# Kernel optimization log

Measured on AMD Instinct MI355X. Metric: run time of the kernel, lower is better.

Reference implementation:

```python
import jax, jax.numpy as jnp
import numpy as np

N_NODES = 100000
N_EDGES = 1600000
IN_DIM, HID, OUT_DIM = 128, 64, 1


def _sage_conv(x, src, dst, wl, wr, b, num_nodes):
    # PyG SAGEConv (aggr='mean', root_weight=True):
    #   out = lin_l(mean_{j in N(i)} x_j) + lin_r(x_i), bias lives in lin_l
    msgs = x[src]                                                  # [E, d] gather
    agg = jax.ops.segment_sum(msgs, dst, num_segments=num_nodes)  # [N, d]
    deg = jax.ops.segment_sum(jnp.ones((src.shape[0],), x.dtype), dst,
                              num_segments=num_nodes)              # [N]
    agg = agg / jnp.maximum(deg, 1.0)[:, None]                     # mean aggregation
    return agg @ wl + x @ wr + b


def setup_inputs() -> dict:
    key = jax.random.key(0)
    ks = jax.random.split(key, 12)
    x = jax.random.normal(ks[0], (N_NODES, IN_DIM), dtype=jnp.float32)
    edge_index = jax.random.randint(ks[1], (2, N_EDGES), 0, N_NODES, dtype=jnp.int64)

    def glorot(k, fan_in, fan_out):
        s = jnp.sqrt(2.0 / (fan_in + fan_out)).astype(jnp.float32)
        return jax.random.normal(k, (fan_in, fan_out), dtype=jnp.float32) * s

    return {
        "x": x,
        "edge_index": edge_index,
        "wl0": glorot(ks[2], IN_DIM, HID), "wr0": glorot(ks[3], IN_DIM, HID),
        "b0": jnp.zeros((HID,), jnp.float32),
        "wl1": glorot(ks[4], HID, HID), "wr1": glorot(ks[5], HID, HID),
        "b1": jnp.zeros((HID,), jnp.float32),
        "wl2": glorot(ks[6], HID, OUT_DIM), "wr2": glorot(ks[7], HID, OUT_DIM),
        "b2": jnp.zeros((OUT_DIM,), jnp.float32),
    }


def reference(x, edge_index, wl0, wr0, b0, wl1, wr1, b1, wl2, wr2, b2):
    src, dst = edge_index[0], edge_index[1]
    n = x.shape[0]
    # layer 0: conv -> relu (dropout is identity in eval mode)
    h = jax.nn.relu(_sage_conv(x, src, dst, wl0, wr0, b0, n))
    # layer 1
    h = jax.nn.relu(_sage_conv(h, src, dst, wl1, wr1, b1, n))
    # final layer + sigmoid
    h = _sage_conv(h, src, dst, wl2, wr2, b2, n)
    return jax.nn.sigmoid(h)
```

## Files before the change

### kernel.cpp

```cpp
#include <hip/hip_runtime.h>
#include <hip/hip_bf16.h>
#include <math.h>


#define SHIFT 7
#define BKT 128
#define CHUNK 4096
#define CAP 4096
#define HSTR 72

typedef __bf16 bf16_t;
typedef bf16_t bf16x8 __attribute__((ext_vector_type(8)));
typedef float f32x4 __attribute__((ext_vector_type(4)));

#define B16LO(u) __uint_as_float((u) << 16)
#define B16HI(u) __uint_as_float((u) & 0xffff0000u)

__global__ __launch_bounds__(256) void scatter_prep(const int* __restrict__ srcv,
                                                    const int* __restrict__ dstv,
                                                    int* __restrict__ bcnt,
                                                    int* __restrict__ bucketed,
                                                    int E, int NB, int nbC,
                                                    const float* __restrict__ wl0,
                                                    const float* __restrict__ wr0,
                                                    const float* __restrict__ wl1,
                                                    const float* __restrict__ wr1,
                                                    bf16_t* __restrict__ w0t,
                                                    bf16_t* __restrict__ w1t) {
    if ((int)blockIdx.x >= nbC) {
        int idx = (blockIdx.x - nbC) * 256 + threadIdx.x;
        if (idx < 128 * 128) {
            int j = idx >> 7, k = idx & 127;
            float v = (j < 64) ? wl0[k * 64 + j] : wr0[k * 64 + (j - 64)];
            w0t[idx] = (bf16_t)v;
        } else if (idx < 128 * 128 + 128 * 64) {
            int i2 = idx - 128 * 128;
            int j = i2 >> 6, k = i2 & 63;
            float v = (j < 64) ? wl1[k * 64 + j] : wr1[k * 64 + (j - 64)];
            w1t[i2] = (bf16_t)v;
        }
        return;
    }
    __shared__ int hist[1024];
    __shared__ int offl[1024];
    __shared__ int basel[1024];
    __shared__ int partial[256];
    __shared__ int posA[CHUNK];
    __shared__ int valA[CHUNK];
    const int t = threadIdx.x;
    for (int i = t; i < NB; i += 256) hist[i] = 0;
    __syncthreads();

    const int cbase = blockIdx.x * CHUNK;
    int bk[CHUNK / 256], rk[CHUNK / 256], vv[CHUNK / 256];
#pragma unroll
    for (int k = 0; k < CHUNK / 256; ++k) {
        int e = cbase + t + k * 256;
        if (e < E) {
            int d = dstv[e];
            int s = srcv[e];
            int b = d >> SHIFT;
            bk[k] = b;
            rk[k] = atomicAdd(&hist[b], 1);
            vv[k] = (s << SHIFT) | (d & (BKT - 1));
        } else {
            bk[k] = -1;
        }
    }
    __syncthreads();

    for (int b = t; b < NB; b += 256) {
        int c = hist[b];
        basel[b] = c ? (b * CAP + atomicAdd(&bcnt[b], c)) : 0;
    }
    {
        int g = t * 4;
        int a0 = (g + 0 < NB) ? hist[g + 0] : 0;
        int a1 = (g + 1 < NB) ? hist[g + 1] : 0;
        int a2 = (g + 2 < NB) ? hist[g + 2] : 0;
        int a3 = (g + 3 < NB) ? hist[g + 3] : 0;
        int sum = a0 + a1 + a2 + a3;
        partial[t] = sum;
        __syncthreads();
        for (int d = 1; d < 256; d <<= 1) {
            int x = (t >= d) ? partial[t - d] : 0;
            __syncthreads();
            partial[t] += x;
            __syncthreads();
        }
        int ex = partial[t] - sum;
        if (g + 0 < NB) offl[g + 0] = ex;
        if (g + 1 < NB) offl[g + 1] = ex + a0;
        if (g + 2 < NB) offl[g + 2] = ex + a0 + a1;
        if (g + 3 < NB) offl[g + 3] = ex + a0 + a1 + a2;
    }
    __syncthreads();

    int nloc = E - cbase;
    if (nloc > CHUNK) nloc = CHUNK;
#pragma unroll
    for (int k = 0; k < CHUNK / 256; ++k) {
        if (bk[k] >= 0) {
            int slot = offl[bk[k]] + rk[k];
            posA[slot] = basel[bk[k]] + rk[k];
            valA[slot] = vv[k];
        }
    }
    __syncthreads();
    for (int j = t; j < nloc; j += 256) bucketed[posA[j]] = valA[j];
}

__global__ __launch_bounds__(256) void sort_gemm0(const int* __restrict__ bucketed,
                                                  const int* __restrict__ bcnt,
                                                  int2* __restrict__ od,
                                                  int* __restrict__ csr, int N, int NB,
                                                  const float* __restrict__ x,
                                                  const bf16_t* __restrict__ w0t,
                                                  bf16_t* __restrict__ y) {
    __shared__ int cnt[BKT];
    __shared__ int sc[BKT];
    __shared__ int cur[BKT];
    const int t = threadIdx.x;

    if ((int)blockIdx.x >= NB) {
        const int bid = blockIdx.x - NB;
        const int lane = t & 63;
        const int wv = t >> 6;
        const int r0 = bid * 64 + wv * 16;
        const int rr = lane & 15;
        const int quad = lane >> 4;
        const int row_store = r0 + rr;
        int row = (row_store < N) ? row_store : (N - 1);

        bf16x8 xf[4];
#pragma unroll
        for (int kk = 0; kk < 4; ++kk) {
            const float* ap = &x[(size_t)row * 128 + kk * 32 + quad * 8];
            float4 f0 = *(const float4*)ap;
            float4 f1 = *(const float4*)(ap + 4);
            union { bf16x8 v; bf16_t h[8]; } u;
            u.h[0] = (bf16_t)f0.x; u.h[1] = (bf16_t)f0.y;
            u.h[2] = (bf16_t)f0.z; u.h[3] = (bf16_t)f0.w;
            u.h[4] = (bf16_t)f1.x; u.h[5] = (bf16_t)f1.y;
            u.h[6] = (bf16_t)f1.z; u.h[7] = (bf16_t)f1.w;
            xf[kk] = u.v;
        }
#pragma unroll
        for (int c = 0; c < 8; ++c) {
            f32x4 acc = {0.f, 0.f, 0.f, 0.f};
#pragma unroll
            for (int kk = 0; kk < 4; ++kk) {
                bf16x8 wf = *(const bf16x8*)&w0t[(size_t)(c * 16 + rr) * 128 + kk * 32 + quad * 8];
                acc = __builtin_amdgcn_mfma_f32_16x16x32_bf16(wf, xf[kk], acc, 0, 0, 0);
            }
            if (row_store < N) {
                union { bf16_t h[4]; uint2 u; } p;
                p.h[0] = (bf16_t)acc[0]; p.h[1] = (bf16_t)acc[1];
                p.h[2] = (bf16_t)acc[2]; p.h[3] = (bf16_t)acc[3];
                *(uint2*)&y[(size_t)row_store * 128 + c * 16 + quad * 4] = p.u;
            }
        }
        return;
    }

    const int b = blockIdx.x;
    const int ebase = b * CAP;
    const int eend = ebase + bcnt[b];
    if (t < BKT) cnt[t] = 0;
    __syncthreads();
    int wreg[CAP / 256];
#pragma unroll
    for (int k = 0; k < CAP / 256; ++k) {
        int i = ebase + t + k * 256;
        if (i < eend) {
            wreg[k] = bucketed[i];
            atomicAdd(&cnt[wreg[k] & (BKT - 1)], 1);
        }
    }
    __syncthreads();
    int v = (t < BKT) ? cnt[t] : 0;
    if (t < BKT) sc[t] = v;
    __syncthreads();
    for (int d = 1; d < BKT; d <<= 1) {
        int xsc = (t < BKT && t >= d) ? sc[t - d] : 0;
        __syncthreads();
        if (t < BKT) sc[t] += xsc;
        __syncthreads();
    }
    if (t < BKT) {
        int ex = sc[t] - v;
        cur[t] = ex;
        int dst = (b << SHIFT) + t;
        if (dst < N) od[dst] = make_int2(ebase + ex, v);
    }
    __syncthreads();
#pragma unroll
    for (int k = 0; k < CAP / 256; ++k) {
        int i = ebase + t + k * 256;
        if (i < eend) {
            int w = wreg[k];
            int p = atomicAdd(&cur[w & (BKT - 1)], 1);
            csr[ebase + p] = w >> SHIFT;
        }
    }
}

__global__ __launch_bounds__(256) void agg0_gemm1(const bf16_t* __restrict__ y,
                                                  const int* __restrict__ csr,
                                                  const int2* __restrict__ od,
                                                  const float* __restrict__ bias,
                                                  const bf16_t* __restrict__ w1t,
                                                  bf16_t* __restrict__ Y, int N) {
    __shared__ bf16_t hlds[64 * HSTR];
    const int t = threadIdx.x;
    const int lane = t & 63;
    const int wv = t >> 6;
    const int oct = lane >> 3;
    const int ch = (lane & 7) * 8;
    const int gbase = blockIdx.x * 64;
    const int n0 = gbase + wv * 16;

    const float4 bv0 = *(const float4*)&bias[ch];
    const float4 bv1 = *(const float4*)&bias[ch + 4];

    int i = n0;
    int2 odc = (i < N) ? od[i] : make_int2(0, 0);
    int sidx = 0;
    if (i < N && lane < odc.y) sidx = csr[odc.x + lane];

    for (int k = 0; k < 16; ++k) {
        const int inext = n0 + k + 1;
        const bool pf = (k < 15) && (inext < N);
        int2 odn = pf ? od[inext] : make_int2(0, 0);

        const int base = odc.x;
        const int d = (i < N) ? odc.y : 0;
        float a0 = 0.f, a1 = 0.f, a2 = 0.f, a3 = 0.f;
        float a4 = 0.f, a5 = 0.f, a6 = 0.f, a7 = 0.f;
        const int nblk = d >> 3;
        const int pm = (nblk < 8) ? nblk : 8;
        int p = 0;
        for (; p + 2 <= pm; p += 2) {
            int s0 = __shfl(sidx, 8 * p + oct);
            int s1 = __shfl(sidx, 8 * p + 8 + oct);
            uint4 v0 = *(const uint4*)&y[(size_t)s0 * 128 + ch];
            uint4 v1 = *(const uint4*)&y[(size_t)s1 * 128 + ch];
            a0 += B16LO(v0.x) + B16LO(v1.x); a1 += B16HI(v0.x) + B16HI(v1.x);
            a2 += B16LO(v0.y) + B16LO(v1.y); a3 += B16HI(v0.y) + B16HI(v1.y);
            a4 += B16LO(v0.z) + B16LO(v1.z); a5 += B16HI(v0.z) + B16HI(v1.z);
            a6 += B16LO(v0.w) + B16LO(v1.w); a7 += B16HI(v0.w) + B16HI(v1.w);
        }
        for (; p < pm; ++p) {
            int s0 = __shfl(sidx, 8 * p + oct);
            uint4 v0 = *(const uint4*)&y[(size_t)s0 * 128 + ch];
            a0 += B16LO(v0.x); a1 += B16HI(v0.x);
            a2 += B16LO(v0.y); a3 += B16HI(v0.y);
            a4 += B16LO(v0.z); a5 += B16HI(v0.z);
            a6 += B16LO(v0.w); a7 += B16HI(v0.w);
        }
        for (; p < nblk; ++p) {
            int s0 = csr[base + 8 * p + oct];
            uint4 v0 = *(const uint4*)&y[(size_t)s0 * 128 + ch];
            a0 += B16LO(v0.x); a1 += B16HI(v0.x);
            a2 += B16LO(v0.y); a3 += B16HI(v0.y);
            a4 += B16LO(v0.z); a5 += B16HI(v0.z);
            a6 += B16LO(v0.w); a7 += B16HI(v0.w);
        }
        {
            int te = 8 * nblk + oct;
            int tec = (te < 64) ? te : 63;
            int s_t = __shfl(sidx, tec);
            if (te < d) {
                int s0 = (te < 64) ? s_t : csr[base + te];
                uint4 v0 = *(const uint4*)&y[(size_t)s0 * 128 + ch];
                a0 += B16LO(v0.x); a1 += B16HI(v0.x);
                a2 += B16LO(v0.y); a3 += B16HI(v0.y);
                a4 += B16LO(v0.z); a5 += B16HI(v0.z);
                a6 += B16LO(v0.w); a7 += B16HI(v0.w);
            }
        }

        int sidxn = 0;
        if (pf && lane < odn.y) sidxn = csr[odn.x + lane];

        a0 += __shfl_xor(a0, 8);  a1 += __shfl_xor(a1, 8);
        a2 += __shfl_xor(a2, 8);  a3 += __shfl_xor(a3, 8);
        a4 += __shfl_xor(a4, 8);  a5 += __shfl_xor(a5, 8);
        a6 += __shfl_xor(a6, 8);  a7 += __shfl_xor(a7, 8);
        a0 += __shfl_xor(a0, 16); a1 += __shfl_xor(a1, 16);
        a2 += __shfl_xor(a2, 16); a3 += __shfl_xor(a3, 16);
        a4 += __shfl_xor(a4, 16); a5 += __shfl_xor(a5, 16);
        a6 += __shfl_xor(a6, 16); a7 += __shfl_xor(a7, 16);
        a0 += __shfl_xor(a0, 32); a1 += __shfl_xor(a1, 32);
        a2 += __shfl_xor(a2, 32); a3 += __shfl_xor(a3, 32);
        a4 += __shfl_xor(a4, 32); a5 += __shfl_xor(a5, 32);
        a6 += __shfl_xor(a6, 32); a7 += __shfl_xor(a7, 32);

        if (i < N) {
            float inv = 1.f / ((d > 0) ? (float)d : 1.f);
            uint4 vs = *(const uint4*)&y[(size_t)i * 128 + 64 + ch];
            float v0 = fmaxf(a0 * inv + B16LO(vs.x) + bv0.x, 0.f);
            float v1 = fmaxf(a1 * inv + B16HI(vs.x) + bv0.y, 0.f);
            float v2 = fmaxf(a2 * inv + B16LO(vs.y) + bv0.z, 0.f);
            float v3 = fmaxf(a3 * inv + B16HI(vs.y) + bv0.w, 0.f);
            float v4 = fmaxf(a4 * inv + B16LO(vs.z) + bv1.x, 0.f);
            float v5 = fmaxf(a5 * inv + B16HI(vs.z) + bv1.y, 0.f);
            float v6 = fmaxf(a6 * inv + B16LO(vs.w) + bv1.z, 0.f);
            float v7 = fmaxf(a7 * inv + B16HI(vs.w) + bv1.w, 0.f);
            if (oct == 0) {
                union { bf16_t b[8]; uint4 u; } pk;
                pk.b[0] = (bf16_t)v0; pk.b[1] = (bf16_t)v1;
                pk.b[2] = (bf16_t)v2; pk.b[3] = (bf16_t)v3;
                pk.b[4] = (bf16_t)v4; pk.b[5] = (bf16_t)v5;
                pk.b[6] = (bf16_t)v6; pk.b[7] = (bf16_t)v7;
                *(uint4*)&hlds[(wv * 16 + k) * HSTR + ch] = pk.u;
            }
        }

        odc = odn;
        sidx = sidxn;
        i = inext;
    }
    __syncthreads();

    const int rr = lane & 15;
    const int quad = lane >> 4;
    const int row_store = gbase + wv * 16 + rr;

    bf16x8 xf[2];
#pragma unroll
    for (int kk = 0; kk < 2; ++kk)
        xf[kk] = *(const bf16x8*)&hlds[(wv * 16 + rr) * HSTR + kk * 32 + quad * 8];

#pragma unroll
    for (int c = 0; c < 8; ++c) {
        f32x4 acc = {0.f, 0.f, 0.f, 0.f};
#pragma unroll
        for (int kk = 0; kk < 2; ++kk) {
            bf16x8 wf = *(const bf16x8*)&w1t[(size_t)(c * 16 + rr) * 64 + kk * 32 + quad * 8];
            acc = __builtin_amdgcn_mfma_f32_16x16x32_bf16(wf, xf[kk], acc, 0, 0, 0);
        }
        if (row_store < N) {
            union { bf16_t h[4]; uint2 u; } p;
            p.h[0] = (bf16_t)acc[0]; p.h[1] = (bf16_t)acc[1];
            p.h[2] = (bf16_t)acc[2]; p.h[3] = (bf16_t)acc[3];
            *(uint2*)&Y[(size_t)row_store * 128 + c * 16 + quad * 4] = p.u;
        }
    }
}

__global__ __launch_bounds__(256) void agg1(const bf16_t* __restrict__ y,
                                            const int* __restrict__ csr,
                                            const int2* __restrict__ od,
                                            const float* __restrict__ bias,
                                            const float* __restrict__ wl2,
                                            const float* __restrict__ wr2,
                                            float* __restrict__ sl,
                                            float* __restrict__ sr, int N) {
    const int lane = threadIdx.x & 63;
    const int oct = lane >> 3;
    const int ch = (lane & 7) * 8;
    const int nw = gridDim.x * 4;

    int i = blockIdx.x * 4 + (threadIdx.x >> 6);
    int2 odc = (i < N) ? od[i] : make_int2(0, 0);
    int sidx = 0;
    if (i < N) sidx = (lane < odc.y) ? csr[odc.x + lane] : 0;

    while (i < N) {
        const int inext = i + nw;
        int2 odn = (inext < N) ? od[inext] : make_int2(0, 0);

        const int base = odc.x;
        const int d = odc.y;
        float a0 = 0.f, a1 = 0.f, a2 = 0.f, a3 = 0.f;
        float a4 = 0.f, a5 = 0.f, a6 = 0.f, a7 = 0.f;
        const int nblk = d >> 3;
        const int pm = (nblk < 8) ? nblk : 8;
        int p = 0;
        for (; p + 2 <= pm; p += 2) {
            int s0 = __shfl(sidx, 8 * p + oct);
            int s1 = __shfl(sidx, 8 * p + 8 + oct);
            uint4 v0 = *(const uint4*)&y[(size_t)s0 * 128 + ch];
            uint4 v1 = *(const uint4*)&y[(size_t)s1 * 128 + ch];
            a0 += B16LO(v0.x) + B16LO(v1.x); a1 += B16HI(v0.x) + B16HI(v1.x);
            a2 += B16LO(v0.y) + B16LO(v1.y); a3 += B16HI(v0.y) + B16HI(v1.y);
            a4 += B16LO(v0.z) + B16LO(v1.z); a5 += B16HI(v0.z) + B16HI(v1.z);
            a6 += B16LO(v0.w) + B16LO(v1.w); a7 += B16HI(v0.w) + B16HI(v1.w);
        }
        for (; p < pm; ++p) {
            int s0 = __shfl(sidx, 8 * p + oct);
            uint4 v0 = *(const uint4*)&y[(size_t)s0 * 128 + ch];
            a0 += B16LO(v0.x); a1 += B16HI(v0.x);
            a2 += B16LO(v0.y); a3 += B16HI(v0.y);
            a4 += B16LO(v0.z); a5 += B16HI(v0.z);
            a6 += B16LO(v0.w); a7 += B16HI(v0.w);
        }
        for (; p < nblk; ++p) {
            int s0 = csr[base + 8 * p + oct];
            uint4 v0 = *(const uint4*)&y[(size_t)s0 * 128 + ch];
            a0 += B16LO(v0.x); a1 += B16HI(v0.x);
            a2 += B16LO(v0.y); a3 += B16HI(v0.y);
            a4 += B16LO(v0.z); a5 += B16HI(v0.z);
            a6 += B16LO(v0.w); a7 += B16HI(v0.w);
        }
        {
            int te = 8 * nblk + oct;
            int tec = (te < 64) ? te : 63;
            int s_t = __shfl(sidx, tec);
            if (te < d) {
                int s0 = (te < 64) ? s_t : csr[base + te];
                uint4 v0 = *(const uint4*)&y[(size_t)s0 * 128 + ch];
                a0 += B16LO(v0.x); a1 += B16HI(v0.x);
                a2 += B16LO(v0.y); a3 += B16HI(v0.y);
                a4 += B16LO(v0.z); a5 += B16HI(v0.z);
                a6 += B16LO(v0.w); a7 += B16HI(v0.w);
            }
        }

        int sidxn = 0;
        if (inext < N) sidxn = (lane < odn.y) ? csr[odn.x + lane] : 0;

        a0 += __shfl_xor(a0, 8);  a1 += __shfl_xor(a1, 8);
        a2 += __shfl_xor(a2, 8);  a3 += __shfl_xor(a3, 8);
        a4 += __shfl_xor(a4, 8);  a5 += __shfl_xor(a5, 8);
        a6 += __shfl_xor(a6, 8);  a7 += __shfl_xor(a7, 8);
        a0 += __shfl_xor(a0, 16); a1 += __shfl_xor(a1, 16);
        a2 += __shfl_xor(a2, 16); a3 += __shfl_xor(a3, 16);
        a4 += __shfl_xor(a4, 16); a5 += __shfl_xor(a5, 16);
        a6 += __shfl_xor(a6, 16); a7 += __shfl_xor(a7, 16);
        a0 += __shfl_xor(a0, 32); a1 += __shfl_xor(a1, 32);
        a2 += __shfl_xor(a2, 32); a3 += __shfl_xor(a3, 32);
        a4 += __shfl_xor(a4, 32); a5 += __shfl_xor(a5, 32);
        a6 += __shfl_xor(a6, 32); a7 += __shfl_xor(a7, 32);

        float inv = 1.f / ((d > 0) ? (float)d : 1.f);
        uint4 vs = *(const uint4*)&y[(size_t)i * 128 + 64 + ch];
        float4 bv0 = *(const float4*)&bias[ch];
        float4 bv1 = *(const float4*)&bias[ch + 4];
        float v0 = fmaxf(a0 * inv + B16LO(vs.x) + bv0.x, 0.f);
        float v1 = fmaxf(a1 * inv + B16HI(vs.x) + bv0.y, 0.f);
        float v2 = fmaxf(a2 * inv + B16LO(vs.y) + bv0.z, 0.f);
        float v3 = fmaxf(a3 * inv + B16HI(vs.y) + bv0.w, 0.f);
        float v4 = fmaxf(a4 * inv + B16LO(vs.z) + bv1.x, 0.f);
        float v5 = fmaxf(a5 * inv + B16HI(vs.z) + bv1.y, 0.f);
        float v6 = fmaxf(a6 * inv + B16LO(vs.w) + bv1.z, 0.f);
        float v7 = fmaxf(a7 * inv + B16HI(vs.w) + bv1.w, 0.f);

        {
            float4 w0 = *(const float4*)&wl2[ch];
            float4 w1 = *(const float4*)&wl2[ch + 4];
            float4 u0 = *(const float4*)&wr2[ch];
            float4 u1 = *(const float4*)&wr2[ch + 4];
            float a = v0 * w0.x + v1 * w0.y + v2 * w0.z + v3 * w0.w +
                      v4 * w1.x + v5 * w1.y + v6 * w1.z + v7 * w1.w;
            float b = v0 * u0.x + v1 * u0.y + v2 * u0.z + v3 * u0.w +
                      v4 * u1.x + v5 * u1.y + v6 * u1.z + v7 * u1.w;
            a += __shfl_xor(a, 1); b += __shfl_xor(b, 1);
            a += __shfl_xor(a, 2); b += __shfl_xor(b, 2);
            a += __shfl_xor(a, 4); b += __shfl_xor(b, 4);
            if (lane == 0) { sl[i] = a; sr[i] = b; }
        }

        odc = odn;
        sidx = sidxn;
        i = inext;
    }
}

__global__ __launch_bounds__(256) void final_k(const float* __restrict__ sl,
                                               const float* __restrict__ sr,
                                               const int* __restrict__ csr,
                                               const int2* __restrict__ od,
                                               const float* __restrict__ b2,
                                               float* __restrict__ out, int N) {
    int wid = blockIdx.x * 4 + (threadIdx.x >> 6);
    if (wid >= N) return;
    const int lane = threadIdx.x & 63;
    const int2 odv = od[wid];
    const int base = odv.x;
    const int d = odv.y;
    float acc = 0.f;
    for (int e = lane; e < d; e += 64) acc += sl[csr[base + e]];
#pragma unroll
    for (int off = 32; off; off >>= 1) acc += __shfl_xor(acc, off);
    if (lane == 0) {
        float m = (d > 0) ? (float)d : 1.f;
        float v = acc / m + sr[wid] + b2[0];
        out[wid] = 1.f / (1.f + expf(-v));
    }
}

extern "C" void kernel_launch(void* const* d_in, const int* in_sizes, int n_in,
                              void* d_out, int out_size, void* d_ws, size_t ws_size,
                              hipStream_t stream) {
    const float* x  = (const float*)d_in[0];
    const int*  ei  = (const int*)d_in[1];
    const float* wl0 = (const float*)d_in[2];
    const float* wr0 = (const float*)d_in[3];
    const float* b0  = (const float*)d_in[4];
    const float* wl1 = (const float*)d_in[5];
    const float* wr1 = (const float*)d_in[6];
    const float* b1  = (const float*)d_in[7];
    const float* wl2 = (const float*)d_in[8];
    const float* wr2 = (const float*)d_in[9];
    const float* b2  = (const float*)d_in[10];
    float* out = (float*)d_out;

    const int E = in_sizes[1] / 2;
    const int N = out_size;
    const int* srcv = ei;
    const int* dstv = ei + E;
    const int NB = (N + BKT - 1) >> SHIFT;

    char* ws = (char*)d_ws;
    size_t o = 0;
    auto take = [&](size_t nbytes) -> void* {
        void* p = ws + o;
        o = (o + nbytes + 255) & ~(size_t)255;
        return p;
    };
    int2* od      = (int2*)take((size_t)N * 8);
    int* bcnt     = (int*)take((size_t)(NB + 2) * 4);
    int* bucketed = (int*)take((size_t)NB * CAP * 4);
    int* csr      = (int*)take((size_t)NB * CAP * 4);
    bf16_t* w0t   = (bf16_t*)take(128 * 128 * 2);
    bf16_t* w1t   = (bf16_t*)take(128 * 64 * 2);
    bf16_t* y     = (bf16_t*)take((size_t)N * 128 * 2);
    bf16_t* y2    = (bf16_t*)take((size_t)N * 128 * 2);
    float* sl     = (float*)take((size_t)N * 4);
    float* sr     = (float*)take((size_t)N * 4);
    (void)ws_size;

    const int nbC = (E + CHUNK - 1) / CHUNK;
    const int nbP = (128 * 128 + 128 * 64 + 255) / 256;
    const int nbW = (N + 3) / 4;
    const int nbG = (N + 63) / 64;
    const int nbA = 2048;

    hipMemsetAsync(bcnt, 0, (size_t)NB * 4, stream);
    scatter_prep<<<nbC + nbP, 256, 0, stream>>>(srcv, dstv, bcnt, bucketed, E, NB, nbC,
                                                wl0, wr0, wl1, wr1, w0t, w1t);
    sort_gemm0<<<NB + nbG, 256, 0, stream>>>(bucketed, bcnt, od, csr, N, NB,
                                             x, w0t, y);

    agg0_gemm1<<<nbG, 256, 0, stream>>>(y, csr, od, b0, w1t, y2, N);
    agg1<<<nbA, 256, 0, stream>>>(y2, csr, od, b1, wl2, wr2, sl, sr, N);
    final_k<<<nbW, 256, 0, stream>>>(sl, sr, csr, od, b2, out, N);
}
```

Measured before the change: 290.2 us.

## Fuse per-bucket sort with layer-0 aggregation and layer-1 GEMM, cache CSR in LDS

The kernel pipeline is reorganized. Weight conversion and the bucket-count zeroing move into a small init kernel that replaces the memset. The layer-0 GEMM now runs in the same launch as the edge scatter. The per-bucket counting sort is fused with layer-0 mean aggregation and the layer-1 MFMA GEMM, so each block builds its 128 destinations' CSR and keeps the first 2560 entries in shared memory for the gather. This removes one launch and the CSR/offset round trip through global memory. In exchange, larger shared memory per block may lower occupancy, and the aggregation now has only NB blocks of parallelism, 128 nodes each.

Measured after the change: 289.7 us. No clear change (-0.2%).

```diff
diff --git a/kernel.cpp b/kernel.cpp
--- a/kernel.cpp
+++ b/kernel.cpp
@@ -7,6 +7,7 @@
 #define BKT 128
 #define CHUNK 4096
 #define CAP 4096
+#define LCAP 2560
 #define HSTR 72
 
 typedef __bf16 bf16_t;
@@ -16,31 +17,90 @@
 #define B16LO(u) __uint_as_float((u) << 16)
 #define B16HI(u) __uint_as_float((u) & 0xffff0000u)
 
-__global__ __launch_bounds__(256) void scatter_prep(const int* __restrict__ srcv,
-                                                    const int* __restrict__ dstv,
-                                                    int* __restrict__ bcnt,
-                                                    int* __restrict__ bucketed,
-                                                    int E, int NB, int nbC,
-                                                    const float* __restrict__ wl0,
-                                                    const float* __restrict__ wr0,
-                                                    const float* __restrict__ wl1,
-                                                    const float* __restrict__ wr1,
-                                                    bf16_t* __restrict__ w0t,
-                                                    bf16_t* __restrict__ w1t) {
+#define ADD8(P, V) { P##0 += B16LO(V.x); P##1 += B16HI(V.x); \
+                     P##2 += B16LO(V.y); P##3 += B16HI(V.y); \
+                     P##4 += B16LO(V.z); P##5 += B16HI(V.z); \
+                     P##6 += B16LO(V.w); P##7 += B16HI(V.w); }
+#define BFLY(P, M) { P##0 += __shfl_xor(P##0, M); P##1 += __shfl_xor(P##1, M); \
+                     P##2 += __shfl_xor(P##2, M); P##3 += __shfl_xor(P##3, M); \
+                     P##4 += __shfl_xor(P##4, M); P##5 += __shfl_xor(P##5, M); \
+                     P##6 += __shfl_xor(P##6, M); P##7 += __shfl_xor(P##7, M); }
+
+__global__ __launch_bounds__(256) void init_k(const float* __restrict__ wl0,
+                                              const float* __restrict__ wr0,
+                                              const float* __restrict__ wl1,
+                                              const float* __restrict__ wr1,
+                                              bf16_t* __restrict__ w0t,
+                                              bf16_t* __restrict__ w1t,
+                                              int* __restrict__ bcnt,
+                                              int NB, int nbP) {
+    if ((int)blockIdx.x >= nbP) {
+        for (int i = threadIdx.x; i < NB; i += 256) bcnt[i] = 0;
+        return;
+    }
+    int idx = blockIdx.x * 256 + threadIdx.x;
+    if (idx < 128 * 128) {
+        int j = idx >> 7, k = idx & 127;
+        float v = (j < 64) ? wl0[k * 64 + j] : wr0[k * 64 + (j - 64)];
+        w0t[idx] = (bf16_t)v;
+    } else if (idx < 128 * 128 + 128 * 64) {
+        int i2 = idx - 128 * 128;
+        int j = i2 >> 6, k = i2 & 63;
+        float v = (j < 64) ? wl1[k * 64 + j] : wr1[k * 64 + (j - 64)];
+        w1t[i2] = (bf16_t)v;
+    }
+}
+
+__global__ __launch_bounds__(256) void scatter_gemm0(const int* __restrict__ srcv,
+                                                     const int* __restrict__ dstv,
+                                                     int* __restrict__ bcnt,
+                                                     int* __restrict__ bucketed,
+                                                     int E, int NB, int nbC,
+                                                     const float* __restrict__ x,
+                                                     const bf16_t* __restrict__ w0t,
+                                                     bf16_t* __restrict__ y, int N) {
     if ((int)blockIdx.x >= nbC) {
-        int idx = (blockIdx.x - nbC) * 256 + threadIdx.x;
-        if (idx < 128 * 128) {
-            int j = idx >> 7, k = idx & 127;
-            float v = (j < 64) ? wl0[k * 64 + j] : wr0[k * 64 + (j - 64)];
-            w0t[idx] = (bf16_t)v;
-        } else if (idx < 128 * 128 + 128 * 64) {
-            int i2 = idx - 128 * 128;
-            int j = i2 >> 6, k = i2 & 63;
-            float v = (j < 64) ? wl1[k * 64 + j] : wr1[k * 64 + (j - 64)];
-            w1t[i2] = (bf16_t)v;
+        const int bid = blockIdx.x - nbC;
+        const int t = threadIdx.x;
+        const int lane = t & 63;
+        const int wv = t >> 6;
+        const int r0 = bid * 64 + wv * 16;
+        const int rr = lane & 15;
+        const int quad = lane >> 4;
+        const int row_store = r0 + rr;
+        int row = (row_store < N) ? row_store : (N - 1);
+
+        bf16x8 xf[4];
+#pragma unroll
+        for (int kk = 0; kk < 4; ++kk) {
+            const float* ap = &x[(size_t)row * 128 + kk * 32 + quad * 8];
+            float4 f0 = *(const float4*)ap;
+            float4 f1 = *(const float4*)(ap + 4);
+            union { bf16x8 v; bf16_t h[8]; } u;
+            u.h[0] = (bf16_t)f0.x; u.h[1] = (bf16_t)f0.y;
+            u.h[2] = (bf16_t)f0.z; u.h[3] = (bf16_t)f0.w;
+            u.h[4] = (bf16_t)f1.x; u.h[5] = (bf16_t)f1.y;
+            u.h[6] = (bf16_t)f1.z; u.h[7] = (bf16_t)f1.w;
+            xf[kk] = u.v;
+        }
+#pragma unroll
+        for (int c = 0; c < 8; ++c) {
+            f32x4 acc = {0.f, 0.f, 0.f, 0.f};
+#pragma unroll
+            for (int kk = 0; kk < 4; ++kk) {
+                bf16x8 wf = *(const bf16x8*)&w0t[(size_t)(c * 16 + rr) * 128 + kk * 32 + quad * 8];
+                acc = __builtin_amdgcn_mfma_f32_16x16x32_bf16(wf, xf[kk], acc, 0, 0, 0);
+            }
+            if (row_store < N) {
+                union { bf16_t h[4]; uint2 u; } p;
+                p.h[0] = (bf16_t)acc[0]; p.h[1] = (bf16_t)acc[1];
+                p.h[2] = (bf16_t)acc[2]; p.h[3] = (bf16_t)acc[3];
+                *(uint2*)&y[(size_t)row_store * 128 + c * 16 + quad * 4] = p.u;
+            }
         }
         return;
     }
+
     __shared__ int hist[1024];
     __shared__ int offl[1024];
     __shared__ int basel[1024];
@@ -83,9 +143,9 @@
         partial[t] = sum;
         __syncthreads();
         for (int d = 1; d < 256; d <<= 1) {
-            int x = (t >= d) ? partial[t - d] : 0;
+            int xsc = (t >= d) ? partial[t - d] : 0;
             __syncthreads();
-            partial[t] += x;
+            partial[t] += xsc;
             __syncthreads();
         }
         int ex = partial[t] - sum;
@@ -110,62 +170,26 @@
     for (int j = t; j < nloc; j += 256) bucketed[posA[j]] = valA[j];
 }
 
-__global__ __launch_bounds__(256) void sort_gemm0(const int* __restrict__ bucketed,
-                                                  const int* __restrict__ bcnt,
-                                                  int2* __restrict__ od,
-                                                  int* __restrict__ csr, int N, int NB,
-                                                  const float* __restrict__ x,
-                                                  const bf16_t* __restrict__ w0t,
-                                                  bf16_t* __restrict__ y) {
+__global__ __launch_bounds__(256) void sort_agg0_gemm1(const int* __restrict__ bucketed,
+                                                       const int* __restrict__ bcnt,
+                                                       int2* __restrict__ od,
+                                                       int* __restrict__ csr,
+                                                       const bf16_t* __restrict__ y,
+                                                       const float* __restrict__ bias,
+                                                       const bf16_t* __restrict__ w1t,
+                                                       bf16_t* __restrict__ y2,
+                                                       int N, int NB) {
     __shared__ int cnt[BKT];
     __shared__ int sc[BKT];
     __shared__ int cur[BKT];
+    __shared__ int lcsr[LCAP];
+    __shared__ bf16_t hlds[BKT * HSTR];
     const int t = threadIdx.x;
-
-    if ((int)blockIdx.x >= NB) {
-        const int bid = blockIdx.x - NB;
-        const int lane = t & 63;
-        const int wv = t >> 6;
-        const int r0 = bid * 64 + wv * 16;
-        const int rr = lane & 15;
-        const int quad = lane >> 4;
-        const int row_store = r0 + rr;
-        int row = (row_store < N) ? row_store : (N - 1);
-
-        bf16x8 xf[4];
-#pragma unroll
-        for (int kk = 0; kk < 4; ++kk) {
-            const float* ap = &x[(size_t)row * 128 + kk * 32 + quad * 8];
-            float4 f0 = *(const float4*)ap;
-            float4 f1 = *(const float4*)(ap + 4);
-            union { bf16x8 v; bf16_t h[8]; } u;
-            u.h[0] = (bf16_t)f0.x; u.h[1] = (bf16_t)f0.y;
-            u.h[2] = (bf16_t)f0.z; u.h[3] = (bf16_t)f0.w;
-            u.h[4] = (bf16_t)f1.x; u.h[5] = (bf16_t)f1.y;
-            u.h[6] = (bf16_t)f1.z; u.h[7] = (bf16_t)f1.w;
-            xf[kk] = u.v;
-        }
-#pragma unroll
-        for (int c = 0; c < 8; ++c) {
-            f32x4 acc = {0.f, 0.f, 0.f, 0.f};
-#pragma unroll
-            for (int kk = 0; kk < 4; ++kk) {
-                bf16x8 wf = *(const bf16x8*)&w0t[(size_t)(c * 16 + rr) * 128 + kk * 32 + quad * 8];
-                acc = __builtin_amdgcn_mfma_f32_16x16x32_bf16(wf, xf[kk], acc, 0, 0, 0);
-            }
-            if (row_store < N) {
-                union { bf16_t h[4]; uint2 u; } p;
-                p.h[0] = (bf16_t)acc[0]; p.h[1] = (bf16_t)acc[1];
-                p.h[2] = (bf16_t)acc[2]; p.h[3] = (bf16_t)acc[3];
-                *(uint2*)&y[(size_t)row_store * 128 + c * 16 + quad * 4] = p.u;
-            }
-        }
-        return;
-    }
-
     const int b = blockIdx.x;
     const int ebase = b * CAP;
-    const int eend = ebase + bcnt[b];
+    const int ecnt = bcnt[b];
+    const int eend = ebase + ecnt;
+
     if (t < BKT) cnt[t] = 0;
     __syncthreads();
     int wreg[CAP / 256];
@@ -200,41 +224,31 @@
         if (i < eend) {
             int w = wreg[k];
             int p = atomicAdd(&cur[w & (BKT - 1)], 1);
-            csr[ebase + p] = w >> SHIFT;
-        }
-    }
-}
-
-__global__ __launch_bounds__(256) void agg0_gemm1(const bf16_t* __restrict__ y,
-                                                  const int* __restrict__ csr,
-                                                  const int2* __restrict__ od,
-                                                  const float* __restrict__ bias,
-                                                  const bf16_t* __restrict__ w1t,
-                                                  bf16_t* __restrict__ Y, int N) {
-    __shared__ bf16_t hlds[64 * HSTR];
-    const int t = threadIdx.x;
+            int s = w >> SHIFT;
+            csr[ebase + p] = s;
+            if (p < LCAP) lcsr[p] = s;
+        }
+    }
+    __syncthreads();
+
     const int lane = t & 63;
     const int wv = t >> 6;
     const int oct = lane >> 3;
     const int ch = (lane & 7) * 8;
-    const int gbase = blockIdx.x * 64;
-    const int n0 = gbase + wv * 16;
-
+    const int gbase = b << SHIFT;
     const float4 bv0 = *(const float4*)&bias[ch];
     const float4 bv1 = *(const float4*)&bias[ch + 4];
 
-    int i = n0;
-    int2 odc = (i < N) ? od[i] : make_int2(0, 0);
-    int sidx = 0;
-    if (i < N && lane < odc.y) sidx = csr[odc.x + lane];
-
-    for (int k = 0; k < 16; ++k) {
-        const int inext = n0 + k + 1;
-        const bool pf = (k < 15) && (inext < N);
-        int2 odn = pf ? od[inext] : make_int2(0, 0);
-
-        const int base = odc.x;
-        const int d = (i < N) ? odc.y : 0;
+    for (int k = 0; k < 32; ++k) {
+        const int n = wv * 32 + k;
+        const int gi = gbase + n;
+        const int d = (gi < N) ? cnt[n] : 0;
+        const int bas = sc[n] - cnt[n];
+        int sidx = 0;
+        if (lane < d) {
+            int slot = bas + lane;
+            sidx = (slot < LCAP) ? lcsr[slot] : csr[ebase + slot];
+        }
         float a0 = 0.f, a1 = 0.f, a2 = 0.f, a3 = 0.f;
         float a4 = 0.f, a5 = 0.f, a6 = 0.f, a7 = 0.f;
         const int nblk = d >> 3;
@@ -245,60 +259,34 @@
             int s1 = __shfl(sidx, 8 * p + 8 + oct);
             uint4 v0 = *(const uint4*)&y[(size_t)s0 * 128 + ch];
             uint4 v1 = *(const uint4*)&y[(size_t)s1 * 128 + ch];
-            a0 += B16LO(v0.x) + B16LO(v1.x); a1 += B16HI(v0.x) + B16HI(v1.x);
-            a2 += B16LO(v0.y) + B16LO(v1.y); a3 += B16HI(v0.y) + B16HI(v1.y);
-            a4 += B16LO(v0.z) + B16LO(v1.z); a5 += B16HI(v0.z) + B16HI(v1.z);
-            a6 += B16LO(v0.w) + B16LO(v1.w); a7 += B16HI(v0.w) + B16HI(v1.w);
+            ADD8(a, v0); ADD8(a, v1);
         }
         for (; p < pm; ++p) {
             int s0 = __shfl(sidx, 8 * p + oct);
             uint4 v0 = *(const uint4*)&y[(size_t)s0 * 128 + ch];
-            a0 += B16LO(v0.x); a1 += B16HI(v0.x);
-            a2 += B16LO(v0.y); a3 += B16HI(v0.y);
-            a4 += B16LO(v0.z); a5 += B16HI(v0.z);
-            a6 += B16LO(v0.w); a7 += B16HI(v0.w);
+            ADD8(a, v0);
         }
         for (; p < nblk; ++p) {
-            int s0 = csr[base + 8 * p + oct];
+            int s0 = csr[ebase + bas + 8 * p + oct];
             uint4 v0 = *(const uint4*)&y[(size_t)s0 * 128 + ch];
-            a0 += B16LO(v0.x); a1 += B16HI(v0.x);
-            a2 += B16LO(v0.y); a3 += B16HI(v0.y);
-            a4 += B16LO(v0.z); a5 += B16HI(v0.z);
-            a6 += B16LO(v0.w); a7 += B16HI(v0.w);
+            ADD8(a, v0);
         }
         {
             int te = 8 * nblk + oct;
             int tec = (te < 64) ? te : 63;
             int s_t = __shfl(sidx, tec);
             if (te < d) {
-                int s0 = (te < 64) ? s_t : csr[base + te];
+                int s0 = (te < 64) ? s_t : csr[ebase + bas + te];
                 uint4 v0 = *(const uint4*)&y[(size_t)s0 * 128 + ch];
-                a0 += B16LO(v0.x); a1 += B16HI(v0.x);
-                a2 += B16LO(v0.y); a3 += B16HI(v0.y);
-                a4 += B16LO(v0.z); a5 += B16HI(v0.z);
-                a6 += B16LO(v0.w); a7 += B16HI(v0.w);
-            }
-        }
-
-        int sidxn = 0;
-        if (pf && lane < odn.y) sidxn = csr[odn.x + lane];
-
-        a0 += __shfl_xor(a0, 8);  a1 += __shfl_xor(a1, 8);
-        a2 += __shfl_xor(a2, 8);  a3 += __shfl_xor(a3, 8);
-        a4 += __shfl_xor(a4, 8);  a5 += __shfl_xor(a5, 8);
-        a6 += __shfl_xor(a6, 8);  a7 += __shfl_xor(a7, 8);
-        a0 += __shfl_xor(a0, 16); a1 += __shfl_xor(a1, 16);
-        a2 += __shfl_xor(a2, 16); a3 += __shfl_xor(a3, 16);
-        a4 += __shfl_xor(a4, 16); a5 += __shfl_xor(a5, 16);
-        a6 += __shfl_xor(a6, 16); a7 += __shfl_xor(a7, 16);
-        a0 += __shfl_xor(a0, 32); a1 += __shfl_xor(a1, 32);
-        a2 += __shfl_xor(a2, 32); a3 += __shfl_xor(a3, 32);
-        a4 += __shfl_xor(a4, 32); a5 += __shfl_xor(a5, 32);
-        a6 += __shfl_xor(a6, 32); a7 += __shfl_xor(a7, 32);
-
-        if (i < N) {
+                ADD8(a, v0);
+            }
+        }
+
+        BFLY(a, 8); BFLY(a, 16); BFLY(a, 32);
+
+        if (gi < N) {
             float inv = 1.f / ((d > 0) ? (float)d : 1.f);
-            uint4 vs = *(const uint4*)&y[(size_t)i * 128 + 64 + ch];
+            uint4 vs = *(const uint4*)&y[(size_t)gi * 128 + 64 + ch];
             float v0 = fmaxf(a0 * inv + B16LO(vs.x) + bv0.x, 0.f);
             float v1 = fmaxf(a1 * inv + B16HI(vs.x) + bv0.y, 0.f);
             float v2 = fmaxf(a2 * inv + B16LO(vs.y) + bv0.z, 0.f);
@@ -308,43 +296,41 @@
             float v6 = fmaxf(a6 * inv + B16LO(vs.w) + bv1.z, 0.f);
             float v7 = fmaxf(a7 * inv + B16HI(vs.w) + bv1.w, 0.f);
             if (oct == 0) {
-                union { bf16_t b[8]; uint4 u; } pk;
-                pk.b[0] = (bf16_t)v0; pk.b[1] = (bf16_t)v1;
-                pk.b[2] = (bf16_t)v2; pk.b[3] = (bf16_t)v3;
-                pk.b[4] = (bf16_t)v4; pk.b[5] = (bf16_t)v5;
-                pk.b[6] = (bf16_t)v6; pk.b[7] = (bf16_t)v7;
-                *(uint4*)&hlds[(wv * 16 + k) * HSTR + ch] = pk.u;
-            }
-        }
-
-        odc = odn;
-        sidx = sidxn;
-        i = inext;
+                union { bf16_t bb[8]; uint4 u; } pk;
+                pk.bb[0] = (bf16_t)v0; pk.bb[1] = (bf16_t)v1;
+                pk.bb[2] = (bf16_t)v2; pk.bb[3] = (bf16_t)v3;
+                pk.bb[4] = (bf16_t)v4; pk.bb[5] = (bf16_t)v5;
+                pk.bb[6] = (bf16_t)v6; pk.bb[7] = (bf16_t)v7;
+                *(uint4*)&hlds[n * HSTR + ch] = pk.u;
+            }
+        }
     }
     __syncthreads();
 
     const int rr = lane & 15;
     const int quad = lane >> 4;
-    const int row_store = gbase + wv * 16 + rr;
-
-    bf16x8 xf[2];
-#pragma unroll
-    for (int kk = 0; kk < 2; ++kk)
-        xf[kk] = *(const bf16x8*)&hlds[(wv * 16 + rr) * HSTR + kk * 32 + quad * 8];
-
-#pragma unroll
-    for (int c = 0; c < 8; ++c) {
-        f32x4 acc = {0.f, 0.f, 0.f, 0.f};
-#pragma unroll
-        for (int kk = 0; kk < 2; ++kk) {
-            bf16x8 wf = *(const bf16x8*)&w1t[(size_t)(c * 16 + rr) * 64 + kk * 32 + quad * 8];
-            acc = __builtin_amdgcn_mfma_f32_16x16x32_bf16(wf, xf[kk], acc, 0, 0, 0);
-        }
-        if (row_store < N) {
-            union { bf16_t h[4]; uint2 u; } p;
-            p.h[0] = (bf16_t)acc[0]; p.h[1] = (bf16_t)acc[1];
-            p.h[2] = (bf16_t)acc[2]; p.h[3] = (bf16_t)acc[3];
-            *(uint2*)&Y[(size_t)row_store * 128 + c * 16 + quad * 4] = p.u;
+#pragma unroll
+    for (int half = 0; half < 2; ++half) {
+        const int rloc = wv * 32 + half * 16 + rr;
+        const int row_store = gbase + rloc;
+        bf16x8 xf[2];
+#pragma unroll
+        for (int kk = 0; kk < 2; ++kk)
+            xf[kk] = *(const bf16x8*)&hlds[rloc * HSTR + kk * 32 + quad * 8];
+#pragma unroll
+        for (int c = 0; c < 8; ++c) {
+            f32x4 acc = {0.f, 0.f, 0.f, 0.f};
+#pragma unroll
+            for (int kk = 0; kk < 2; ++kk) {
+                bf16x8 wf = *(const bf16x8*)&w1t[(size_t)(c * 16 + rr) * 64 + kk * 32 + quad * 8];
+                acc = __builtin_amdgcn_mfma_f32_16x16x32_bf16(wf, xf[kk], acc, 0, 0, 0);
+            }
+            if (row_store < N) {
+                union { bf16_t h[4]; uint2 u; } p;
+                p.h[0] = (bf16_t)acc[0]; p.h[1] = (bf16_t)acc[1];
+                p.h[2] = (bf16_t)acc[2]; p.h[3] = (bf16_t)acc[3];
+                *(uint2*)&y2[(size_t)row_store * 128 + c * 16 + quad * 4] = p.u;
+            }
         }
     }
 }
@@ -383,26 +369,17 @@
             int s1 = __shfl(sidx, 8 * p + 8 + oct);
             uint4 v0 = *(const uint4*)&y[(size_t)s0 * 128 + ch];
             uint4 v1 = *(const uint4*)&y[(size_t)s1 * 128 + ch];
-            a0 += B16LO(v0.x) + B16LO(v1.x); a1 += B16HI(v0.x) + B16HI(v1.x);
-            a2 += B16LO(v0.y) + B16LO(v1.y); a3 += B16HI(v0.y) + B16HI(v1.y);
-            a4 += B16LO(v0.z) + B16LO(v1.z); a5 += B16HI(v0.z) + B16HI(v1.z);
-            a6 += B16LO(v0.w) + B16LO(v1.w); a7 += B16HI(v0.w) + B16HI(v1.w);
+            ADD8(a, v0); ADD8(a, v1);
         }
         for (; p < pm; ++p) {
             int s0 = __shfl(sidx, 8 * p + oct);
             uint4 v0 = *(const uint4*)&y[(size_t)s0 * 128 + ch];
-            a0 += B16LO(v0.x); a1 += B16HI(v0.x);
-            a2 += B16LO(v0.y); a3 += B16HI(v0.y);
-            a4 += B16LO(v0.z); a5 += B16HI(v0.z);
-            a6 += B16LO(v0.w); a7 += B16HI(v0.w);
+            ADD8(a, v0);
         }
         for (; p < nblk; ++p) {
             int s0 = csr[base + 8 * p + oct];
             uint4 v0 = *(const uint4*)&y[(size_t)s0 * 128 + ch];
-            a0 += B16LO(v0.x); a1 += B16HI(v0.x);
-            a2 += B16LO(v0.y); a3 += B16HI(v0.y);
-            a4 += B16LO(v0.z); a5 += B16HI(v0.z);
-            a6 += B16LO(v0.w); a7 += B16HI(v0.w);
+            ADD8(a, v0);
         }
         {
             int te = 8 * nblk + oct;
@@ -411,28 +388,14 @@
             if (te < d) {
                 int s0 = (te < 64) ? s_t : csr[base + te];
                 uint4 v0 = *(const uint4*)&y[(size_t)s0 * 128 + ch];
-                a0 += B16LO(v0.x); a1 += B16HI(v0.x);
-                a2 += B16LO(v0.y); a3 += B16HI(v0.y);
-                a4 += B16LO(v0.z); a5 += B16HI(v0.z);
-                a6 += B16LO(v0.w); a7 += B16HI(v0.w);
+                ADD8(a, v0);
             }
         }
 
         int sidxn = 0;
         if (inext < N) sidxn = (lane < odn.y) ? csr[odn.x + lane] : 0;
 
-        a0 += __shfl_xor(a0, 8);  a1 += __shfl_xor(a1, 8);
-        a2 += __shfl_xor(a2, 8);  a3 += __shfl_xor(a3, 8);
-        a4 += __shfl_xor(a4, 8);  a5 += __shfl_xor(a5, 8);
-        a6 += __shfl_xor(a6, 8);  a7 += __shfl_xor(a7, 8);
-        a0 += __shfl_xor(a0, 16); a1 += __shfl_xor(a1, 16);
-        a2 += __shfl_xor(a2, 16); a3 += __shfl_xor(a3, 16);
-        a4 += __shfl_xor(a4, 16); a5 += __shfl_xor(a5, 16);
-        a6 += __shfl_xor(a6, 16); a7 += __shfl_xor(a7, 16);
-        a0 += __shfl_xor(a0, 32); a1 += __shfl_xor(a1, 32);
-        a2 += __shfl_xor(a2, 32); a3 += __shfl_xor(a3, 32);
-        a4 += __shfl_xor(a4, 32); a5 += __shfl_xor(a5, 32);
-        a6 += __shfl_xor(a6, 32); a7 += __shfl_xor(a7, 32);
+        BFLY(a, 8); BFLY(a, 16); BFLY(a, 32);
 
         float inv = 1.f / ((d > 0) ? (float)d : 1.f);
         uint4 vs = *(const uint4*)&y[(size_t)i * 128 + 64 + ch];
@@ -538,13 +501,12 @@
     const int nbG = (N + 63) / 64;
     const int nbA = 2048;
 
-    hipMemsetAsync(bcnt, 0, (size_t)NB * 4, stream);
-    scatter_prep<<<nbC + nbP, 256, 0, stream>>>(srcv, dstv, bcnt, bucketed, E, NB, nbC,
-                                                wl0, wr0, wl1, wr1, w0t, w1t);
-    sort_gemm0<<<NB + nbG, 256, 0, stream>>>(bucketed, bcnt, od, csr, N, NB,
-                                             x, w0t, y);
-
-    agg0_gemm1<<<nbG, 256, 0, stream>>>(y, csr, od, b0, w1t, y2, N);
+    init_k<<<nbP + 1, 256, 0, stream>>>(wl0, wr0, wl1, wr1, w0t, w1t, bcnt, NB, nbP);
+    scatter_gemm0<<<nbC + nbG, 256, 0, stream>>>(srcv, dstv, bcnt, bucketed, E, NB, nbC,
+                                                 x, w0t, y, N);
+
+    sort_agg0_gemm1<<<NB, 256, 0, stream>>>(bucketed, bcnt, od, csr, y, b0, w1t,
+                                            y2, N, NB);
     agg1<<<nbA, 256, 0, stream>>>(y2, csr, od, b1, wl2, wr2, sl, sr, N);
     final_k<<<nbW, 256, 0, stream>>>(sl, sr, csr, od, b2, out, N);
 }
```
